# Kernel tuning notes

Hardware: AMD Instinct MI355X
Metric: run time of the kernel (lower is better)

Reference implementation:

```python
import jax, jax.numpy as jnp
import numpy as np

B, S, D, H = 2, 1024, 1024, 2048
E = 8          # hash_size: number of expert FFNs
DICT = 32000   # dict_size: vocab for the hash map


def setup_inputs() -> dict:
    key = jax.random.key(0)
    k = jax.random.split(key, 7)
    x = jax.random.normal(k[0], (B, S, D), dtype=jnp.float32)
    orig_input = jax.random.randint(k[1], (B, S), 0, DICT, dtype=jnp.int32)
    # random token -> expert hash map (random.randrange(0, hashsize) in original)
    hash_map = jax.random.randint(k[2], (DICT,), 0, E, dtype=jnp.int32)
    # torch Linear weights are [out, in]; xavier_uniform for weights, default uniform for biases
    lim1 = float(np.sqrt(6.0 / (D + H)))
    lim2 = float(np.sqrt(6.0 / (H + D)))
    W1 = jax.random.uniform(k[3], (E, H, D), minval=-lim1, maxval=lim1, dtype=jnp.float32)
    b1 = jax.random.uniform(k[4], (E, H), minval=-1.0 / np.sqrt(D), maxval=1.0 / np.sqrt(D), dtype=jnp.float32)
    W2 = jax.random.uniform(k[5], (E, D, H), minval=-lim2, maxval=lim2, dtype=jnp.float32)
    b2 = jax.random.uniform(k[6], (E, D), minval=-1.0 / np.sqrt(H), maxval=1.0 / np.sqrt(H), dtype=jnp.float32)
    return {"x": x, "orig_input": orig_input, "hash_map": hash_map,
            "W1": W1, "b1": b1, "W2": W2, "b2": b2}


def reference(x, orig_input, hash_map, W1, b1, W2, b2):
    # expert id per token (hash routing)
    e = hash_map[orig_input]                      # [B, S]
    out = jnp.zeros_like(x)
    # loop over the small fixed set of experts; each iteration is a dense
    # 2-layer FFN, with the token->expert mask selecting which outputs land.
    # (relu_dropout = 0 -> identity; eval-mode semantics)
    for i in range(E):
        h = jax.nn.relu(jnp.einsum('bsd,hd->bsh', x, W1[i]) + b1[i])   # [B,S,H]
        y = jnp.einsum('bsh,dh->bsd', h, W2[i]) + b2[i]                # [B,S,D]
        out = jnp.where((e == i)[..., None], y, out)
    return out
```

## Files before the change

kernel.cpp:

```cpp
#include <hip/hip_runtime.h>
#include <hip/hip_bf16.h>
#include <stdint.h>

#define TOKENS 2048
#define DD 1024
#define HH 2048
#define NE 8
#define RP_CAP 3072
#define BM 64
#define BN 64
#define BK 64

typedef float f32x4 __attribute__((ext_vector_type(4)));
typedef short bf16x8 __attribute__((ext_vector_type(8)));
typedef unsigned int u32;

__device__ __forceinline__ unsigned short f2bf(float f) {
    union { float f; u32 u; } v; v.f = f;
    u32 u = v.u;
    return (unsigned short)((u + 0x7fffu + ((u >> 16) & 1u)) >> 16);
}

__global__ __launch_bounds__(256) void k_route(const int* __restrict__ orig,
                                               const int* __restrict__ hmap,
                                               int* __restrict__ hdr) {
    __shared__ int s_e[TOKENS];
    __shared__ int s_cnt[NE];
    __shared__ int s_off[NE];
    int tid = threadIdx.x;
    if (tid < NE) s_cnt[tid] = 0;
    __syncthreads();
    for (int t = tid; t < TOKENS; t += 256) {
        int e = hmap[orig[t]];
        s_e[t] = e;
        atomicAdd(&s_cnt[e], 1);
    }
    __syncthreads();
    if (tid == 0) {
        int run = 0;
        for (int e = 0; e < NE; ++e) {
            s_off[e] = run;
            hdr[e] = s_cnt[e];
            hdr[8 + e] = run;
            run += ((s_cnt[e] + BM - 1) / BM) * BM;
        }
        hdr[16] = run;
    }
    __syncthreads();
    int* perm = hdr + 64;
    for (int r = tid; r < RP_CAP; r += 256) perm[r] = -1;
    if (tid < NE) s_cnt[tid] = 0;
    __syncthreads();
    for (int t = tid; t < TOKENS; t += 256) {
        int e = s_e[t];
        int pos = s_off[e] + atomicAdd(&s_cnt[e], 1);
        perm[pos] = t;
    }
}

__global__ __launch_bounds__(256) void k_gather(const float* __restrict__ x,
                                                const int* __restrict__ hdr,
                                                unsigned short* __restrict__ xp) {
    int r = blockIdx.x;
    int t = hdr[64 + r];
    int tid = threadIdx.x;
    ushort4* dst = (ushort4*)(xp + (size_t)r * DD);
    if (t >= 0) {
        const float4* src = (const float4*)(x + (size_t)t * DD);
        float4 v = src[tid];
        ushort4 o;
        o.x = f2bf(v.x); o.y = f2bf(v.y); o.z = f2bf(v.z); o.w = f2bf(v.w);
        dst[tid] = o;
    } else {
        ushort4 z; z.x = 0; z.y = 0; z.z = 0; z.w = 0;
        dst[tid] = z;
    }
}

template<int KDIM, int NDIM, bool L2EPI>
__global__ __launch_bounds__(256, 4) void k_gemm(const unsigned short* __restrict__ A,
                                                 const float* __restrict__ W,
                                                 const float* __restrict__ bias,
                                                 const int* __restrict__ hdr,
                                                 unsigned short* __restrict__ hout,
                                                 float* __restrict__ out) {
    int total = hdr[16];
    int row0 = blockIdx.y * BM;
    if (row0 >= total) return;
    int e = 0;
#pragma unroll
    for (int i = 1; i < NE; ++i)
        if (row0 >= hdr[8 + i]) e = i;

    int n0 = blockIdx.x * BN;
    const float* We = W + (size_t)e * NDIM * KDIM;
    const float* be = bias + (size_t)e * NDIM;

    __shared__ __align__(16) unsigned short As[2 * BM * BK];
    __shared__ __align__(16) unsigned short Bs[2 * BN * BK];

    int tid = threadIdx.x;
    int w = tid >> 6, lane = tid & 63;
    int wr = w >> 1, wc = w & 1;
    int fr = lane & 15, hi = lane >> 4;

    f32x4 acc[2][2];
#pragma unroll
    for (int m = 0; m < 2; ++m)
#pragma unroll
        for (int n = 0; n < 2; ++n) acc[m][n] = f32x4{0.f, 0.f, 0.f, 0.f};

    float4 bvA[4], bvB[4];

    auto STAGE_A = [&](int buf, int k0) {
#pragma unroll
        for (int j = 0; j < 2; ++j) {
            int c = j * 256 + tid;
            int row = c >> 3;
            int slot = c & 7;
            int gslot = slot ^ (row & 7);
            const unsigned short* gp = A + (size_t)(row0 + row) * KDIM + k0 + gslot * 8;
            unsigned short* lp = (unsigned short*)As + buf * (BM * BK) + j * 2048 + w * 512;
            __builtin_amdgcn_global_load_lds((const __attribute__((address_space(1))) u32*)gp,
                                             (__attribute__((address_space(3))) u32*)lp, 16, 0, 0);
        }
    };
    auto B_LOAD = [&](float4 (&bv)[4], int k0) {
#pragma unroll
        for (int jr = 0; jr < 2; ++jr) {
            int c = jr * 256 + tid;
            int row = c >> 3;
            int cl = c & 7;
            const float4* gp = (const float4*)(We + (size_t)(n0 + row) * KDIM + k0 + cl * 8);
            bv[jr * 2]     = gp[0];
            bv[jr * 2 + 1] = gp[1];
        }
    };
    auto B_WRITE = [&](const float4 (&bv)[4], int buf) {
        unsigned short* Bb = Bs + buf * (BN * BK);
#pragma unroll
        for (int jr = 0; jr < 2; ++jr) {
            int c = jr * 256 + tid;
            int row = c >> 3;
            int cl = c & 7;
            float4 v0 = bv[jr * 2], v1 = bv[jr * 2 + 1];
            union { bf16x8 v; unsigned short s[8]; } o;
            o.s[0] = f2bf(v0.x); o.s[1] = f2bf(v0.y); o.s[2] = f2bf(v0.z); o.s[3] = f2bf(v0.w);
            o.s[4] = f2bf(v1.x); o.s[5] = f2bf(v1.y); o.s[6] = f2bf(v1.z); o.s[7] = f2bf(v1.w);
            int sp = cl ^ (row & 7);
            *(bf16x8*)&Bb[row * 64 + sp * 8] = o.v;
        }
    };
    auto COMPUTE = [&](int buf) {
        const unsigned short* Ab = As + buf * (BM * BK);
        const unsigned short* Bb = Bs + buf * (BN * BK);
#pragma unroll
        for (int kk = 0; kk < BK; kk += 32) {
            bf16x8 af[2], bfr[2];
#pragma unroll
            for (int m = 0; m < 2; ++m) {
                int rr = wr * 32 + m * 16 + fr;
                int idx = (rr * 64 + kk + hi * 8) ^ ((rr & 7) << 3);
                af[m] = *(const bf16x8*)&Ab[idx];
            }
#pragma unroll
            for (int n = 0; n < 2; ++n) {
                int cn = wc * 32 + n * 16 + fr;
                int idx = (cn * 64 + kk + hi * 8) ^ ((cn & 7) << 3);
                bfr[n] = *(const bf16x8*)&Bb[idx];
            }
#pragma unroll
            for (int m = 0; m < 2; ++m)
#pragma unroll
                for (int n = 0; n < 2; ++n)
                    acc[m][n] = __builtin_amdgcn_mfma_f32_16x16x32_bf16(af[m], bfr[n], acc[m][n], 0, 0, 0);
        }
    };

    constexpr int NT = KDIM / BK;

#define WAIT_KEEP6 asm volatile("s_waitcnt vmcnt(6) lgkmcnt(0)" ::: "memory")
#define WAIT_ALL   asm volatile("s_waitcnt vmcnt(0) lgkmcnt(0)" ::: "memory")
#define BARRIER    do { __builtin_amdgcn_s_barrier(); asm volatile("" ::: "memory"); } while (0)

    STAGE_A(0, 0);
    B_LOAD(bvA, 0);
    B_LOAD(bvB, BK);
    B_WRITE(bvA, 0);
    WAIT_KEEP6;
    BARRIER;

    for (int t = 0; t < NT; t += 2) {
        STAGE_A(1, (t + 1) * BK);
        if (t + 2 < NT) B_LOAD(bvA, (t + 2) * BK);
        COMPUTE(0);
        B_WRITE(bvB, 1);
        if (t + 2 < NT) WAIT_KEEP6; else WAIT_ALL;
        BARRIER;
        if (t + 2 < NT) {
            STAGE_A(0, (t + 2) * BK);
            if (t + 3 < NT) B_LOAD(bvB, (t + 3) * BK);
            COMPUTE(1);
            B_WRITE(bvA, 0);
            if (t + 3 < NT) WAIT_KEEP6; else WAIT_ALL;
            BARRIER;
        } else {
            COMPUTE(1);
        }
    }
#undef WAIT_KEEP6
#undef WAIT_ALL
#undef BARRIER

    const int* perm = hdr + 64;
    int rbase = row0 + wr * 32 + hi * 4;
    int cbase = n0 + wc * 32 + fr;
    if constexpr (!L2EPI) {
#pragma unroll
        for (int n = 0; n < 2; ++n) {
            int cg = cbase + n * 16;
            float bvv = be[cg];
#pragma unroll
            for (int m = 0; m < 2; ++m) {
                int rg = rbase + m * 16;
#pragma unroll
                for (int r = 0; r < 4; ++r) {
                    float v = acc[m][n][r] + bvv;
                    v = v > 0.f ? v : 0.f;
                    hout[(size_t)(rg + r) * NDIM + cg] = f2bf(v);
                }
            }
        }
    } else {
        float bvv[2];
#pragma unroll
        for (int n = 0; n < 2; ++n) bvv[n] = be[cbase + n * 16];
#pragma unroll
        for (int m = 0; m < 2; ++m) {
            int rg = rbase + m * 16;
#pragma unroll
            for (int r = 0; r < 4; ++r) {
                int t = perm[rg + r];
                if (t < 0) continue;
                float* op = out + (size_t)t * DD;
#pragma unroll
                for (int n = 0; n < 2; ++n)
                    op[cbase + n * 16] = acc[m][n][r] + bvv[n];
            }
        }
    }
}

extern "C" void kernel_launch(void* const* d_in, const int* in_sizes, int n_in,
                              void* d_out, int out_size, void* d_ws, size_t ws_size,
                              hipStream_t stream) {
    const float* x    = (const float*)d_in[0];
    const int*   orig = (const int*)d_in[1];
    const int*   hmap = (const int*)d_in[2];
    const float* W1   = (const float*)d_in[3];
    const float* b1   = (const float*)d_in[4];
    const float* W2   = (const float*)d_in[5];
    const float* b2   = (const float*)d_in[6];
    float* out = (float*)d_out;

    int* hdr = (int*)d_ws;
    unsigned short* xp   = (unsigned short*)((char*)d_ws + 16384);
    unsigned short* hbuf = (unsigned short*)((char*)d_ws + 16384 + (size_t)RP_CAP * DD * 2);

    k_route<<<1, 256, 0, stream>>>(orig, hmap, hdr);
    k_gather<<<RP_CAP, 256, 0, stream>>>(x, hdr, xp);
    k_gemm<DD, HH, false><<<dim3(HH / BN, RP_CAP / BM), 256, 0, stream>>>(xp, W1, b1, hdr, hbuf, nullptr);
    k_gemm<HH, DD, true><<<dim3(DD / BN, RP_CAP / BM), 256, 0, stream>>>(hbuf, W2, b2, hdr, nullptr, out);
}
```

Baseline: 82.23 us.

## Widen GEMM N-tile via multiple B subtiles per block to reuse A

Each GEMM block now computes NG adjacent 64-column subtiles (4 for the first layer, 2 for the second), sharing the A tile across them. This cuts redundant A loads and block count. The pipeline changes from a two-deep register prefetch of B to a single-step prefetch with a full vmcnt(0) wait each iteration. Register and LDS use per block go up, and launch bounds are lowered. The weaker overlap and lower occupancy could offset the reuse gain.

```diff
diff --git a/kernel.cpp b/kernel.cpp
--- a/kernel.cpp
+++ b/kernel.cpp
@@ -77,13 +77,13 @@
     }
 }
 
-template<int KDIM, int NDIM, bool L2EPI>
-__global__ __launch_bounds__(256, 4) void k_gemm(const unsigned short* __restrict__ A,
-                                                 const float* __restrict__ W,
-                                                 const float* __restrict__ bias,
-                                                 const int* __restrict__ hdr,
-                                                 unsigned short* __restrict__ hout,
-                                                 float* __restrict__ out) {
+template<int KDIM, int NDIM, int NG, int MINW, bool L2EPI>
+__global__ __launch_bounds__(256, MINW) void k_gemm(const unsigned short* __restrict__ A,
+                                                    const float* __restrict__ W,
+                                                    const float* __restrict__ bias,
+                                                    const int* __restrict__ hdr,
+                                                    unsigned short* __restrict__ hout,
+                                                    float* __restrict__ out) {
     int total = hdr[16];
     int row0 = blockIdx.y * BM;
     if (row0 >= total) return;
@@ -92,25 +92,29 @@
     for (int i = 1; i < NE; ++i)
         if (row0 >= hdr[8 + i]) e = i;
 
-    int n0 = blockIdx.x * BN;
+    int n0 = blockIdx.x * (BN * NG);
     const float* We = W + (size_t)e * NDIM * KDIM;
     const float* be = bias + (size_t)e * NDIM;
 
-    __shared__ __align__(16) unsigned short As[2 * BM * BK];
-    __shared__ __align__(16) unsigned short Bs[2 * BN * BK];
+    constexpr int ASZ = BM * BK;
+    constexpr int BSZ = BN * BK;
+    __shared__ __align__(16) unsigned short As[2 * ASZ];
+    __shared__ __align__(16) unsigned short Bs[2 * NG * BSZ];
 
     int tid = threadIdx.x;
     int w = tid >> 6, lane = tid & 63;
     int wr = w >> 1, wc = w & 1;
     int fr = lane & 15, hi = lane >> 4;
 
-    f32x4 acc[2][2];
-#pragma unroll
-    for (int m = 0; m < 2; ++m)
-#pragma unroll
-        for (int n = 0; n < 2; ++n) acc[m][n] = f32x4{0.f, 0.f, 0.f, 0.f};
-
-    float4 bvA[4], bvB[4];
+    f32x4 acc[NG][2][2];
+#pragma unroll
+    for (int s = 0; s < NG; ++s)
+#pragma unroll
+        for (int m = 0; m < 2; ++m)
+#pragma unroll
+            for (int n = 0; n < 2; ++n) acc[s][m][n] = f32x4{0.f, 0.f, 0.f, 0.f};
+
+    float4 bv[NG][4];
 
     auto STAGE_A = [&](int buf, int k0) {
 #pragma unroll
@@ -120,43 +124,48 @@
             int slot = c & 7;
             int gslot = slot ^ (row & 7);
             const unsigned short* gp = A + (size_t)(row0 + row) * KDIM + k0 + gslot * 8;
-            unsigned short* lp = (unsigned short*)As + buf * (BM * BK) + j * 2048 + w * 512;
+            unsigned short* lp = (unsigned short*)As + buf * ASZ + j * 2048 + w * 512;
             __builtin_amdgcn_global_load_lds((const __attribute__((address_space(1))) u32*)gp,
                                              (__attribute__((address_space(3))) u32*)lp, 16, 0, 0);
         }
     };
-    auto B_LOAD = [&](float4 (&bv)[4], int k0) {
-#pragma unroll
-        for (int jr = 0; jr < 2; ++jr) {
-            int c = jr * 256 + tid;
-            int row = c >> 3;
-            int cl = c & 7;
-            const float4* gp = (const float4*)(We + (size_t)(n0 + row) * KDIM + k0 + cl * 8);
-            bv[jr * 2]     = gp[0];
-            bv[jr * 2 + 1] = gp[1];
-        }
-    };
-    auto B_WRITE = [&](const float4 (&bv)[4], int buf) {
-        unsigned short* Bb = Bs + buf * (BN * BK);
-#pragma unroll
-        for (int jr = 0; jr < 2; ++jr) {
-            int c = jr * 256 + tid;
-            int row = c >> 3;
-            int cl = c & 7;
-            float4 v0 = bv[jr * 2], v1 = bv[jr * 2 + 1];
-            union { bf16x8 v; unsigned short s[8]; } o;
-            o.s[0] = f2bf(v0.x); o.s[1] = f2bf(v0.y); o.s[2] = f2bf(v0.z); o.s[3] = f2bf(v0.w);
-            o.s[4] = f2bf(v1.x); o.s[5] = f2bf(v1.y); o.s[6] = f2bf(v1.z); o.s[7] = f2bf(v1.w);
-            int sp = cl ^ (row & 7);
-            *(bf16x8*)&Bb[row * 64 + sp * 8] = o.v;
-        }
-    };
-    auto COMPUTE = [&](int buf) {
-        const unsigned short* Ab = As + buf * (BM * BK);
-        const unsigned short* Bb = Bs + buf * (BN * BK);
+    auto B_LOAD_ALL = [&](int k0) {
+#pragma unroll
+        for (int s = 0; s < NG; ++s) {
+#pragma unroll
+            for (int jr = 0; jr < 2; ++jr) {
+                int c = jr * 256 + tid;
+                int row = c >> 3;
+                int cl = c & 7;
+                const float4* gp = (const float4*)(We + (size_t)(n0 + s * BN + row) * KDIM + k0 + cl * 8);
+                bv[s][jr * 2]     = gp[0];
+                bv[s][jr * 2 + 1] = gp[1];
+            }
+        }
+    };
+    auto B_WRITE_ALL = [&](int buf) {
+#pragma unroll
+        for (int s = 0; s < NG; ++s) {
+            unsigned short* Bb = Bs + (buf * NG + s) * BSZ;
+#pragma unroll
+            for (int jr = 0; jr < 2; ++jr) {
+                int c = jr * 256 + tid;
+                int row = c >> 3;
+                int cl = c & 7;
+                float4 v0 = bv[s][jr * 2], v1 = bv[s][jr * 2 + 1];
+                union { bf16x8 v; unsigned short sv[8]; } o;
+                o.sv[0] = f2bf(v0.x); o.sv[1] = f2bf(v0.y); o.sv[2] = f2bf(v0.z); o.sv[3] = f2bf(v0.w);
+                o.sv[4] = f2bf(v1.x); o.sv[5] = f2bf(v1.y); o.sv[6] = f2bf(v1.z); o.sv[7] = f2bf(v1.w);
+                int sp = cl ^ (row & 7);
+                *(bf16x8*)&Bb[row * 64 + sp * 8] = o.v;
+            }
+        }
+    };
+    auto COMPUTE_ALL = [&](int buf) {
+        const unsigned short* Ab = As + buf * ASZ;
 #pragma unroll
         for (int kk = 0; kk < BK; kk += 32) {
-            bf16x8 af[2], bfr[2];
+            bf16x8 af[2];
 #pragma unroll
             for (int m = 0; m < 2; ++m) {
                 int rr = wr * 32 + m * 16 + fr;
@@ -164,88 +173,88 @@
                 af[m] = *(const bf16x8*)&Ab[idx];
             }
 #pragma unroll
-            for (int n = 0; n < 2; ++n) {
-                int cn = wc * 32 + n * 16 + fr;
-                int idx = (cn * 64 + kk + hi * 8) ^ ((cn & 7) << 3);
-                bfr[n] = *(const bf16x8*)&Bb[idx];
-            }
-#pragma unroll
-            for (int m = 0; m < 2; ++m)
-#pragma unroll
-                for (int n = 0; n < 2; ++n)
-                    acc[m][n] = __builtin_amdgcn_mfma_f32_16x16x32_bf16(af[m], bfr[n], acc[m][n], 0, 0, 0);
+            for (int s = 0; s < NG; ++s) {
+                const unsigned short* Bb = Bs + (buf * NG + s) * BSZ;
+                bf16x8 bfr[2];
+#pragma unroll
+                for (int n = 0; n < 2; ++n) {
+                    int cn = wc * 32 + n * 16 + fr;
+                    int idx = (cn * 64 + kk + hi * 8) ^ ((cn & 7) << 3);
+                    bfr[n] = *(const bf16x8*)&Bb[idx];
+                }
+#pragma unroll
+                for (int m = 0; m < 2; ++m)
+#pragma unroll
+                    for (int n = 0; n < 2; ++n)
+                        acc[s][m][n] = __builtin_amdgcn_mfma_f32_16x16x32_bf16(af[m], bfr[n], acc[s][m][n], 0, 0, 0);
+            }
         }
     };
 
     constexpr int NT = KDIM / BK;
 
-#define WAIT_KEEP6 asm volatile("s_waitcnt vmcnt(6) lgkmcnt(0)" ::: "memory")
-#define WAIT_ALL   asm volatile("s_waitcnt vmcnt(0) lgkmcnt(0)" ::: "memory")
-#define BARRIER    do { __builtin_amdgcn_s_barrier(); asm volatile("" ::: "memory"); } while (0)
+#define WAIT_ALL0 asm volatile("s_waitcnt vmcnt(0) lgkmcnt(0)" ::: "memory")
+#define BARRIER   do { __builtin_amdgcn_s_barrier(); asm volatile("" ::: "memory"); } while (0)
 
     STAGE_A(0, 0);
-    B_LOAD(bvA, 0);
-    B_LOAD(bvB, BK);
-    B_WRITE(bvA, 0);
-    WAIT_KEEP6;
+    B_LOAD_ALL(0);
+    B_WRITE_ALL(0);
+    WAIT_ALL0;
     BARRIER;
 
-    for (int t = 0; t < NT; t += 2) {
-        STAGE_A(1, (t + 1) * BK);
-        if (t + 2 < NT) B_LOAD(bvA, (t + 2) * BK);
-        COMPUTE(0);
-        B_WRITE(bvB, 1);
-        if (t + 2 < NT) WAIT_KEEP6; else WAIT_ALL;
-        BARRIER;
-        if (t + 2 < NT) {
-            STAGE_A(0, (t + 2) * BK);
-            if (t + 3 < NT) B_LOAD(bvB, (t + 3) * BK);
-            COMPUTE(1);
-            B_WRITE(bvA, 0);
-            if (t + 3 < NT) WAIT_KEEP6; else WAIT_ALL;
+    for (int t = 0; t < NT; ++t) {
+        int buf = t & 1;
+        if (t + 1 < NT) {
+            STAGE_A(buf ^ 1, (t + 1) * BK);
+            B_LOAD_ALL((t + 1) * BK);
+        }
+        COMPUTE_ALL(buf);
+        if (t + 1 < NT) {
+            B_WRITE_ALL(buf ^ 1);
+            WAIT_ALL0;
             BARRIER;
-        } else {
-            COMPUTE(1);
-        }
-    }
-#undef WAIT_KEEP6
-#undef WAIT_ALL
+        }
+    }
+#undef WAIT_ALL0
 #undef BARRIER
 
     const int* perm = hdr + 64;
     int rbase = row0 + wr * 32 + hi * 4;
-    int cbase = n0 + wc * 32 + fr;
-    if constexpr (!L2EPI) {
-#pragma unroll
-        for (int n = 0; n < 2; ++n) {
-            int cg = cbase + n * 16;
-            float bvv = be[cg];
+#pragma unroll
+    for (int s = 0; s < NG; ++s) {
+        int cbase = n0 + s * BN + wc * 32 + fr;
+        if constexpr (!L2EPI) {
+#pragma unroll
+            for (int n = 0; n < 2; ++n) {
+                int cg = cbase + n * 16;
+                float bvv = be[cg];
+#pragma unroll
+                for (int m = 0; m < 2; ++m) {
+                    int rg = rbase + m * 16;
+#pragma unroll
+                    for (int r = 0; r < 4; ++r) {
+                        float v = acc[s][m][n][r] + bvv;
+                        v = v > 0.f ? v : 0.f;
+                        hout[(size_t)(rg + r) * NDIM + cg] = f2bf(v);
+                    }
+                }
+            }
+        } else {
+            float bvv[2];
+#pragma unroll
+            for (int n = 0; n < 2; ++n) bvv[n] = be[cbase + n * 16];
 #pragma unroll
             for (int m = 0; m < 2; ++m) {
                 int rg = rbase + m * 16;
 #pragma unroll
                 for (int r = 0; r < 4; ++r) {
-                    float v = acc[m][n][r] + bvv;
-                    v = v > 0.f ? v : 0.f;
-                    hout[(size_t)(rg + r) * NDIM + cg] = f2bf(v);
+                    int tk = perm[rg + r];
+                    if (tk < 0) continue;
+                    float* op = out + (size_t)tk * DD;
+#pragma unroll
+                    for (int n = 0; n < 2; ++n)
+                        op[cbase + n * 16] = acc[s][m][n][r] + bvv[n];
                 }
-            }
-        }
-    } else {
-        float bvv[2];
-#pragma unroll
-        for (int n = 0; n < 2; ++n) bvv[n] = be[cbase + n * 16];
-#pragma unroll
-        for (int m = 0; m < 2; ++m) {
-            int rg = rbase + m * 16;
-#pragma unroll
-            for (int r = 0; r < 4; ++r) {
-                int t = perm[rg + r];
-                if (t < 0) continue;
-                float* op = out + (size_t)t * DD;
-#pragma unroll
-                for (int n = 0; n < 2; ++n)
-                    op[cbase + n * 16] = acc[m][n][r] + bvv[n];
             }
         }
     }
@@ -269,6 +278,6 @@
 
     k_route<<<1, 256, 0, stream>>>(orig, hmap, hdr);
     k_gather<<<RP_CAP, 256, 0, stream>>>(x, hdr, xp);
-    k_gemm<DD, HH, false><<<dim3(HH / BN, RP_CAP / BM), 256, 0, stream>>>(xp, W1, b1, hdr, hbuf, nullptr);
-    k_gemm<HH, DD, true><<<dim3(DD / BN, RP_CAP / BM), 256, 0, stream>>>(hbuf, W2, b2, hdr, nullptr, out);
-}
+    k_gemm<DD, HH, 4, 2, false><<<dim3(HH / (BN * 4), RP_CAP / BM), 256, 0, stream>>>(xp, W1, b1, hdr, hbuf, nullptr);
+    k_gemm<HH, DD, 2, 3, true><<<dim3(DD / (BN * 2), RP_CAP / BM), 256, 0, stream>>>(hbuf, W2, b2, hdr, nullptr, out);
+}
```

Result: slower. 109.8 us (+33.5%).

## Stage fp32 weights directly to LDS with triple-buffered async pipeline

Applied to the files above, without the earlier changes.

The weight tiles are no longer loaded into registers, converted to bf16 and written to LDS. They are now copied as fp32 straight into LDS with global_load_lds, and the bf16 conversion happens at fragment-read time in the compute loop. The double buffer becomes a three-stage rotating ring, prefetching two tiles ahead with one barrier per iteration. This cuts register pressure and VGPR round-trips for B and deepens the prefetch. In exchange, LDS per block roughly doubles, occupancy is lowered to 2 blocks, and the conversion work is repeated per wave on every read.

```diff
diff --git a/kernel.cpp b/kernel.cpp
--- a/kernel.cpp
+++ b/kernel.cpp
@@ -78,7 +78,7 @@
 }
 
 template<int KDIM, int NDIM, bool L2EPI>
-__global__ __launch_bounds__(256, 4) void k_gemm(const unsigned short* __restrict__ A,
+__global__ __launch_bounds__(256, 2) void k_gemm(const unsigned short* __restrict__ A,
                                                  const float* __restrict__ W,
                                                  const float* __restrict__ bias,
                                                  const int* __restrict__ hdr,
@@ -96,8 +96,10 @@
     const float* We = W + (size_t)e * NDIM * KDIM;
     const float* be = bias + (size_t)e * NDIM;
 
-    __shared__ __align__(16) unsigned short As[2 * BM * BK];
-    __shared__ __align__(16) unsigned short Bs[2 * BN * BK];
+    constexpr int ASZ = BM * BK;
+    constexpr int BSZ = BN * BK;
+    __shared__ __align__(16) unsigned short As[3 * ASZ];
+    __shared__ __align__(16) float          Bs[3 * BSZ];
 
     int tid = threadIdx.x;
     int w = tid >> 6, lane = tid & 63;
@@ -110,9 +112,7 @@
 #pragma unroll
         for (int n = 0; n < 2; ++n) acc[m][n] = f32x4{0.f, 0.f, 0.f, 0.f};
 
-    float4 bvA[4], bvB[4];
-
-    auto STAGE_A = [&](int buf, int k0) {
+    auto STAGE = [&](int aoff, int boff, int k0) {
 #pragma unroll
         for (int j = 0; j < 2; ++j) {
             int c = j * 256 + tid;
@@ -120,40 +120,25 @@
             int slot = c & 7;
             int gslot = slot ^ (row & 7);
             const unsigned short* gp = A + (size_t)(row0 + row) * KDIM + k0 + gslot * 8;
-            unsigned short* lp = (unsigned short*)As + buf * (BM * BK) + j * 2048 + w * 512;
+            unsigned short* lp = (unsigned short*)As + aoff + j * 2048 + w * 512;
             __builtin_amdgcn_global_load_lds((const __attribute__((address_space(1))) u32*)gp,
                                              (__attribute__((address_space(3))) u32*)lp, 16, 0, 0);
         }
+#pragma unroll
+        for (int j = 0; j < 4; ++j) {
+            int c = j * 256 + tid;
+            int row = c >> 4;
+            int slot = c & 15;
+            int gslot = slot ^ (row & 15);
+            const float* gp = We + (size_t)(n0 + row) * KDIM + k0 + gslot * 4;
+            float* lp = Bs + boff + j * 1024 + w * 256;
+            __builtin_amdgcn_global_load_lds((const __attribute__((address_space(1))) u32*)gp,
+                                             (__attribute__((address_space(3))) u32*)lp, 16, 0, 0);
+        }
     };
-    auto B_LOAD = [&](float4 (&bv)[4], int k0) {
-#pragma unroll
-        for (int jr = 0; jr < 2; ++jr) {
-            int c = jr * 256 + tid;
-            int row = c >> 3;
-            int cl = c & 7;
-            const float4* gp = (const float4*)(We + (size_t)(n0 + row) * KDIM + k0 + cl * 8);
-            bv[jr * 2]     = gp[0];
-            bv[jr * 2 + 1] = gp[1];
-        }
-    };
-    auto B_WRITE = [&](const float4 (&bv)[4], int buf) {
-        unsigned short* Bb = Bs + buf * (BN * BK);
-#pragma unroll
-        for (int jr = 0; jr < 2; ++jr) {
-            int c = jr * 256 + tid;
-            int row = c >> 3;
-            int cl = c & 7;
-            float4 v0 = bv[jr * 2], v1 = bv[jr * 2 + 1];
-            union { bf16x8 v; unsigned short s[8]; } o;
-            o.s[0] = f2bf(v0.x); o.s[1] = f2bf(v0.y); o.s[2] = f2bf(v0.z); o.s[3] = f2bf(v0.w);
-            o.s[4] = f2bf(v1.x); o.s[5] = f2bf(v1.y); o.s[6] = f2bf(v1.z); o.s[7] = f2bf(v1.w);
-            int sp = cl ^ (row & 7);
-            *(bf16x8*)&Bb[row * 64 + sp * 8] = o.v;
-        }
-    };
-    auto COMPUTE = [&](int buf) {
-        const unsigned short* Ab = As + buf * (BM * BK);
-        const unsigned short* Bb = Bs + buf * (BN * BK);
+    auto COMPUTE = [&](int aoff, int boff) {
+        const unsigned short* Ab = As + aoff;
+        const float* Bb = Bs + boff;
 #pragma unroll
         for (int kk = 0; kk < BK; kk += 32) {
             bf16x8 af[2], bfr[2];
@@ -166,8 +151,14 @@
 #pragma unroll
             for (int n = 0; n < 2; ++n) {
                 int cn = wc * 32 + n * 16 + fr;
-                int idx = (cn * 64 + kk + hi * 8) ^ ((cn & 7) << 3);
-                bfr[n] = *(const bf16x8*)&Bb[idx];
+                int s0 = (kk + hi * 8) >> 2;
+                int xr = cn & 15;
+                const f32x4 v0 = *(const f32x4*)&Bb[cn * 64 + ((s0)     ^ xr) * 4];
+                const f32x4 v1 = *(const f32x4*)&Bb[cn * 64 + ((s0 + 1) ^ xr) * 4];
+                union { bf16x8 v; unsigned short s[8]; } o;
+                o.s[0] = f2bf(v0[0]); o.s[1] = f2bf(v0[1]); o.s[2] = f2bf(v0[2]); o.s[3] = f2bf(v0[3]);
+                o.s[4] = f2bf(v1[0]); o.s[5] = f2bf(v1[1]); o.s[6] = f2bf(v1[2]); o.s[7] = f2bf(v1[3]);
+                bfr[n] = o.v;
             }
 #pragma unroll
             for (int m = 0; m < 2; ++m)
@@ -179,37 +170,30 @@
 
     constexpr int NT = KDIM / BK;
 
-#define WAIT_KEEP6 asm volatile("s_waitcnt vmcnt(6) lgkmcnt(0)" ::: "memory")
-#define WAIT_ALL   asm volatile("s_waitcnt vmcnt(0) lgkmcnt(0)" ::: "memory")
-#define BARRIER    do { __builtin_amdgcn_s_barrier(); asm volatile("" ::: "memory"); } while (0)
-
-    STAGE_A(0, 0);
-    B_LOAD(bvA, 0);
-    B_LOAD(bvB, BK);
-    B_WRITE(bvA, 0);
-    WAIT_KEEP6;
+#define WAIT6   do { asm volatile("s_waitcnt vmcnt(6) lgkmcnt(0)" ::: "memory"); \
+                     __builtin_amdgcn_sched_barrier(0); } while (0)
+#define WAIT0   do { asm volatile("s_waitcnt vmcnt(0) lgkmcnt(0)" ::: "memory"); \
+                     __builtin_amdgcn_sched_barrier(0); } while (0)
+#define BARRIER do { __builtin_amdgcn_s_barrier(); asm volatile("" ::: "memory"); } while (0)
+
+    int a0 = 0, a1 = ASZ, a2 = 2 * ASZ;
+    int b0 = 0, b1 = BSZ, b2 = 2 * BSZ;
+
+    STAGE(a0, b0, 0);
+    STAGE(a1, b1, BK);
+    WAIT6;
     BARRIER;
 
-    for (int t = 0; t < NT; t += 2) {
-        STAGE_A(1, (t + 1) * BK);
-        if (t + 2 < NT) B_LOAD(bvA, (t + 2) * BK);
-        COMPUTE(0);
-        B_WRITE(bvB, 1);
-        if (t + 2 < NT) WAIT_KEEP6; else WAIT_ALL;
-        BARRIER;
-        if (t + 2 < NT) {
-            STAGE_A(0, (t + 2) * BK);
-            if (t + 3 < NT) B_LOAD(bvB, (t + 3) * BK);
-            COMPUTE(1);
-            B_WRITE(bvA, 0);
-            if (t + 3 < NT) WAIT_KEEP6; else WAIT_ALL;
-            BARRIER;
-        } else {
-            COMPUTE(1);
-        }
-    }
-#undef WAIT_KEEP6
-#undef WAIT_ALL
+    for (int t = 0; t < NT; ++t) {
+        if (t + 2 < NT) STAGE(a2, b2, (t + 2) * BK);
+        COMPUTE(a0, b0);
+        if (t + 2 < NT)      { WAIT6; BARRIER; }
+        else if (t + 1 < NT) { WAIT0; BARRIER; }
+        int ta = a0; a0 = a1; a1 = a2; a2 = ta;
+        int tb = b0; b0 = b1; b1 = b2; b2 = tb;
+    }
+#undef WAIT6
+#undef WAIT0
 #undef BARRIER
 
     const int* perm = hdr + 64;
@@ -240,9 +224,9 @@
             int rg = rbase + m * 16;
 #pragma unroll
             for (int r = 0; r < 4; ++r) {
-                int t = perm[rg + r];
-                if (t < 0) continue;
-                float* op = out + (size_t)t * DD;
+                int tk = perm[rg + r];
+                if (tk < 0) continue;
+                float* op = out + (size_t)tk * DD;
 #pragma unroll
                 for (int n = 0; n < 2; ++n)
                     op[cbase + n * 16] = acc[m][n][r] + bvv[n];
```

After: 141.6 us. +72.2%, slower.
